# Kernel optimization log

Hardware: AMD Instinct MI355X
Metric: run time of the kernel (lower is better)

Reference implementation:

```python
import jax, jax.numpy as jnp
import numpy as np

EPS = 1e-12  # tf.math.l2_normalize epsilon

def _l2_normalize(v, axis):
    sq = jnp.sum(v * v, axis=axis, keepdims=True)
    return v * jax.lax.rsqrt(jnp.maximum(sq, EPS))

def setup_inputs() -> dict:
    key = jax.random.key(0)
    k1, k2, k3 = jax.random.split(key, 3)
    B, H, Wd, Cin, K = 16, 64, 64, 512, 64  # K == dim (required by the source's broadcast)
    x = jax.random.normal(k1, (B, H, Wd, Cin), dtype=jnp.float32)
    W = jax.random.normal(k2, (Cin, K), dtype=jnp.float32) * (1.0 / np.sqrt(Cin))
    b = jnp.zeros((K,), dtype=jnp.float32)
    C = jax.random.uniform(k3, (1, 1, 1, K, K), dtype=jnp.float32)  # [1,1,1,dim,clusters]
    return {"x": x, "W": W, "b": b, "C": C}

def reference(x, W, b, C):
    # 1x1 conv: per-pixel linear projection to cluster logits. NOTE: the
    # original code overwrites x with the conv output, so the VLAD residual
    # is built from these logits, not the input features (faithful to source).
    f = jnp.einsum('bhwc,ck->bhwk', x, W) + b            # [B,H,W,K]
    s = jax.nn.softmax(f, axis=-1)                        # soft assignment over clusters
    # a: [B,H,W,1,K], residual: [B,H,W,dim,K] with dim==K
    v = s[..., None, :] * (f[..., :, None] + C)           # [B,H,W,dim,K]
    v = jnp.sum(v, axis=(1, 2))                           # [B,dim,K]
    v = jnp.transpose(v, (0, 2, 1))                       # [B,K,dim]
    # postnorm=True: intra-normalize per cluster, then global L2 of flattened
    v = _l2_normalize(v, axis=-1)
    flat = v.reshape(v.shape[0], -1)                      # [B, K*dim]
    return _l2_normalize(flat, axis=-1)
```

## Files before the change

### kernel.cpp

```cpp
#include <hip/hip_runtime.h>
#include <hip/hip_bf16.h>

#define NB 16
#define HW 4096
#define CIN 512
#define KCL 64
#define BP 128
#define NCHUNK 32
#define PSTRIDE 136

typedef short s16x8 __attribute__((ext_vector_type(8)));
typedef int   i32x4 __attribute__((ext_vector_type(4)));
typedef float f32x4 __attribute__((ext_vector_type(4)));

__device__ __forceinline__ unsigned short f2bf(float f) {
    unsigned u = __builtin_bit_cast(unsigned, f);
    u += 0x7fffu + ((u >> 16) & 1u);
    return (unsigned short)(u >> 16);
}

__device__ __forceinline__ unsigned pk2(float lo, float hi) {
    __hip_bfloat162 h = __float22bfloat162_rn(make_float2(lo, hi));
    unsigned r;
    __builtin_memcpy(&r, &h, 4);
    return r;
}

__global__ void vlad_prep(const float* __restrict__ Wm, float* __restrict__ A_g,
                          unsigned short* __restrict__ Wt_g)
{
    const int i = blockIdx.x * 256 + threadIdx.x;
    if (i < NB * KCL * KCL + NB * KCL) A_g[i] = 0.f;
    if (i < CIN * KCL) {
        const int c = i >> 6;
        const int n = i & 63;
        Wt_g[n * 512 + c] = f2bf(Wm[i]);
    }
}

__global__ __launch_bounds__(256, 4) void vlad_main(
    const float* __restrict__ x, const unsigned short* __restrict__ Wt_g,
    const float* __restrict__ bv, float* __restrict__ A_g,
    float* __restrict__ sumS_g)
{
    __shared__ unsigned short ft[KCL * PSTRIDE];
    __shared__ unsigned short st[KCL * PSTRIDE];

    const int t = threadIdx.x;
    const int b = blockIdx.x >> 5;
    const int chunk = blockIdx.x & 31;
    const int pb = b * HW + chunk * BP;

    const int wid = t >> 6;
    const int lane = t & 63;
    const int col = lane & 15;
    const int g = lane >> 4;
    const int wpix = pb + wid * 32;

    f32x4 acc[2][4];
#pragma unroll
    for (int mt = 0; mt < 2; ++mt)
#pragma unroll
        for (int nt = 0; nt < 4; ++nt) acc[mt][nt] = (f32x4){0.f, 0.f, 0.f, 0.f};

    const float* xr0 = x + (size_t)(wpix + col) * CIN + g * 8;
    const float* xr1 = xr0 + 16 * CIN;
    const unsigned short* wbase = Wt_g + col * 512 + g * 8;

#pragma unroll
    for (int kk = 0; kk < 16; ++kk) {
        const int k0 = kk * 32;
        const float4 u00 = *(const float4*)(xr0 + k0);
        const float4 u01 = *(const float4*)(xr0 + k0 + 4);
        const float4 u10 = *(const float4*)(xr1 + k0);
        const float4 u11 = *(const float4*)(xr1 + k0 + 4);
        s16x8 wf[4];
#pragma unroll
        for (int nt = 0; nt < 4; ++nt)
            wf[nt] = *(const s16x8*)(wbase + nt * (16 * 512) + k0);
        const i32x4 a0i = {(int)pk2(u00.x, u00.y), (int)pk2(u00.z, u00.w),
                           (int)pk2(u01.x, u01.y), (int)pk2(u01.z, u01.w)};
        const i32x4 a1i = {(int)pk2(u10.x, u10.y), (int)pk2(u10.z, u10.w),
                           (int)pk2(u11.x, u11.y), (int)pk2(u11.z, u11.w)};
        const s16x8 a0 = __builtin_bit_cast(s16x8, a0i);
        const s16x8 a1 = __builtin_bit_cast(s16x8, a1i);
#pragma unroll
        for (int nt = 0; nt < 4; ++nt) {
            acc[0][nt] = __builtin_amdgcn_mfma_f32_16x16x32_bf16(a0, wf[nt], acc[0][nt], 0, 0, 0);
            acc[1][nt] = __builtin_amdgcn_mfma_f32_16x16x32_bf16(a1, wf[nt], acc[1][nt], 0, 0, 0);
        }
    }

    float bj[4];
#pragma unroll
    for (int nt = 0; nt < 4; ++nt) bj[nt] = bv[nt * 16 + col];
    float ssum[4] = {0.f, 0.f, 0.f, 0.f};

#pragma unroll
    for (int mt = 0; mt < 2; ++mt)
#pragma unroll
        for (int r = 0; r < 4; ++r) {
            float v0 = acc[mt][0][r] + bj[0];
            float v1 = acc[mt][1][r] + bj[1];
            float v2 = acc[mt][2][r] + bj[2];
            float v3 = acc[mt][3][r] + bj[3];
            float m = fmaxf(fmaxf(v0, v1), fmaxf(v2, v3));
            m = fmaxf(m, __shfl_xor(m, 1));
            m = fmaxf(m, __shfl_xor(m, 2));
            m = fmaxf(m, __shfl_xor(m, 4));
            m = fmaxf(m, __shfl_xor(m, 8));
            const float e0 = __expf(v0 - m);
            const float e1 = __expf(v1 - m);
            const float e2 = __expf(v2 - m);
            const float e3 = __expf(v3 - m);
            float lsum = e0 + e1 + e2 + e3;
            lsum += __shfl_xor(lsum, 1);
            lsum += __shfl_xor(lsum, 2);
            lsum += __shfl_xor(lsum, 4);
            lsum += __shfl_xor(lsum, 8);
            const float rl = 1.0f / lsum;
            const float s0 = e0 * rl, s1 = e1 * rl, s2 = e2 * rl, s3 = e3 * rl;
            ssum[0] += s0; ssum[1] += s1; ssum[2] += s2; ssum[3] += s3;
            const int p = wid * 32 + mt * 16 + g * 4 + r;
            ft[(col)      * PSTRIDE + p] = f2bf(v0);
            ft[(col + 16) * PSTRIDE + p] = f2bf(v1);
            ft[(col + 32) * PSTRIDE + p] = f2bf(v2);
            ft[(col + 48) * PSTRIDE + p] = f2bf(v3);
            st[(col)      * PSTRIDE + p] = f2bf(s0);
            st[(col + 16) * PSTRIDE + p] = f2bf(s1);
            st[(col + 32) * PSTRIDE + p] = f2bf(s2);
            st[(col + 48) * PSTRIDE + p] = f2bf(s3);
        }

#pragma unroll
    for (int nt = 0; nt < 4; ++nt) {
        ssum[nt] += __shfl_xor(ssum[nt], 16);
        ssum[nt] += __shfl_xor(ssum[nt], 32);
    }
    if (g == 0) {
#pragma unroll
        for (int nt = 0; nt < 4; ++nt)
            atomicAdd(sumS_g + b * KCL + nt * 16 + col, ssum[nt]);
    }
    __syncthreads();

    f32x4 acc2[4];
#pragma unroll
    for (int nt = 0; nt < 4; ++nt) acc2[nt] = (f32x4){0.f, 0.f, 0.f, 0.f};

    const unsigned short* fta = ft + (wid * 16 + col) * PSTRIDE + g * 8;
#pragma unroll
    for (int kk = 0; kk < 4; ++kk) {
        const s16x8 af = *(const s16x8*)(fta + kk * 32);
#pragma unroll
        for (int nt = 0; nt < 4; ++nt) {
            const s16x8 bf = *(const s16x8*)(st + (nt * 16 + col) * PSTRIDE + kk * 32 + g * 8);
            acc2[nt] = __builtin_amdgcn_mfma_f32_16x16x32_bf16(af, bf, acc2[nt], 0, 0, 0);
        }
    }

    float* Ab = A_g + b * (KCL * KCL);
#pragma unroll
    for (int nt = 0; nt < 4; ++nt)
#pragma unroll
        for (int r = 0; r < 4; ++r)
            atomicAdd(Ab + (wid * 16 + g * 4 + r) * KCL + nt * 16 + col, acc2[nt][r]);
}

__global__ __launch_bounds__(256) void vlad_finalize(
    const float* __restrict__ A_g, const float* __restrict__ sumS_g,
    const float* __restrict__ Cm, float* __restrict__ out)
{
    __shared__ float red[4];
    const int b = blockIdx.x;
    const int t = threadIdx.x;
    const int k = t >> 2;
    const int dg = t & 3;
    const float sS = sumS_g[b * 64 + k];
    float v[16];
    float ssq = 0.f;
#pragma unroll
    for (int i = 0; i < 16; ++i) {
        const int d = dg * 16 + i;
        const float val = A_g[((size_t)b * 64 + d) * 64 + k] + Cm[d * 64 + k] * sS;
        v[i] = val;
        ssq += val * val;
    }
    ssq += __shfl_xor(ssq, 1);
    ssq += __shfl_xor(ssq, 2);
    const float rn = rsqrtf(fmaxf(ssq, 1e-12f));
    float gpart = 0.f;
#pragma unroll
    for (int i = 0; i < 16; ++i) {
        v[i] *= rn;
        gpart += v[i] * v[i];
    }
#pragma unroll
    for (int m = 1; m < 64; m <<= 1) gpart += __shfl_xor(gpart, m);
    if ((t & 63) == 0) red[t >> 6] = gpart;
    __syncthreads();
    const float gsq = red[0] + red[1] + red[2] + red[3];
    const float gr = rsqrtf(fmaxf(gsq, 1e-12f));
    float* o = out + (size_t)b * 4096 + k * 64 + dg * 16;
#pragma unroll
    for (int i = 0; i < 16; ++i) o[i] = v[i] * gr;
}

extern "C" void kernel_launch(void* const* d_in, const int* in_sizes, int n_in,
                              void* d_out, int out_size, void* d_ws, size_t ws_size,
                              hipStream_t stream)
{
    const float* x  = (const float*)d_in[0];
    const float* Wm = (const float*)d_in[1];
    const float* bv = (const float*)d_in[2];
    const float* Cm = (const float*)d_in[3];

    float* A_g = (float*)d_ws;
    float* sumS_g = A_g + NB * KCL * KCL;
    unsigned short* Wt_g = (unsigned short*)(sumS_g + NB * KCL);

    const int nz = NB * KCL * KCL + NB * KCL;
    vlad_prep<<<(nz + 255) / 256, 256, 0, stream>>>(Wm, A_g, Wt_g);
    vlad_main<<<NB * NCHUNK, 256, 0, stream>>>(x, Wt_g, bv, A_g, sumS_g);
    vlad_finalize<<<NB, 256, 0, stream>>>(A_g, sumS_g, Cm, (float*)d_out);
}
```

Measured before the change: 208.7 us.

## Halve pixels per block, double grid, and vectorize LDS stores of logits/softmax

Each block now handles 64 pixels instead of 128, so each wave computes one 16-row MFMA tile instead of two and the grid doubles to 1024 blocks. This is meant to raise parallelism and occupancy for the memory-bound projection and cut register use. The per-element bf16 LDS stores are also replaced by packed 8-byte stores. The cost is twice as many global atomicAdds into the per-batch 64x64 accumulator and into sumS.

```diff
diff --git a/kernel.cpp b/kernel.cpp
--- a/kernel.cpp
+++ b/kernel.cpp
@@ -5,9 +5,9 @@
 #define HW 4096
 #define CIN 512
 #define KCL 64
-#define BP 128
-#define NCHUNK 32
-#define PSTRIDE 136
+#define BP 64
+#define NCHUNK 64
+#define PSTRIDE 72
 
 typedef short s16x8 __attribute__((ext_vector_type(8)));
 typedef int   i32x4 __attribute__((ext_vector_type(4)));
@@ -47,24 +47,21 @@
     __shared__ unsigned short st[KCL * PSTRIDE];
 
     const int t = threadIdx.x;
-    const int b = blockIdx.x >> 5;
-    const int chunk = blockIdx.x & 31;
+    const int b = blockIdx.x >> 6;
+    const int chunk = blockIdx.x & 63;
     const int pb = b * HW + chunk * BP;
 
     const int wid = t >> 6;
     const int lane = t & 63;
     const int col = lane & 15;
     const int g = lane >> 4;
-    const int wpix = pb + wid * 32;
-
-    f32x4 acc[2][4];
-#pragma unroll
-    for (int mt = 0; mt < 2; ++mt)
-#pragma unroll
-        for (int nt = 0; nt < 4; ++nt) acc[mt][nt] = (f32x4){0.f, 0.f, 0.f, 0.f};
+    const int wpix = pb + wid * 16;
+
+    f32x4 acc[4];
+#pragma unroll
+    for (int nt = 0; nt < 4; ++nt) acc[nt] = (f32x4){0.f, 0.f, 0.f, 0.f};
 
     const float* xr0 = x + (size_t)(wpix + col) * CIN + g * 8;
-    const float* xr1 = xr0 + 16 * CIN;
     const unsigned short* wbase = Wt_g + col * 512 + g * 8;
 
 #pragma unroll
@@ -72,65 +69,59 @@
         const int k0 = kk * 32;
         const float4 u00 = *(const float4*)(xr0 + k0);
         const float4 u01 = *(const float4*)(xr0 + k0 + 4);
-        const float4 u10 = *(const float4*)(xr1 + k0);
-        const float4 u11 = *(const float4*)(xr1 + k0 + 4);
         s16x8 wf[4];
 #pragma unroll
         for (int nt = 0; nt < 4; ++nt)
             wf[nt] = *(const s16x8*)(wbase + nt * (16 * 512) + k0);
         const i32x4 a0i = {(int)pk2(u00.x, u00.y), (int)pk2(u00.z, u00.w),
                            (int)pk2(u01.x, u01.y), (int)pk2(u01.z, u01.w)};
-        const i32x4 a1i = {(int)pk2(u10.x, u10.y), (int)pk2(u10.z, u10.w),
-                           (int)pk2(u11.x, u11.y), (int)pk2(u11.z, u11.w)};
         const s16x8 a0 = __builtin_bit_cast(s16x8, a0i);
-        const s16x8 a1 = __builtin_bit_cast(s16x8, a1i);
-#pragma unroll
-        for (int nt = 0; nt < 4; ++nt) {
-            acc[0][nt] = __builtin_amdgcn_mfma_f32_16x16x32_bf16(a0, wf[nt], acc[0][nt], 0, 0, 0);
-            acc[1][nt] = __builtin_amdgcn_mfma_f32_16x16x32_bf16(a1, wf[nt], acc[1][nt], 0, 0, 0);
-        }
+#pragma unroll
+        for (int nt = 0; nt < 4; ++nt)
+            acc[nt] = __builtin_amdgcn_mfma_f32_16x16x32_bf16(a0, wf[nt], acc[nt], 0, 0, 0);
     }
 
     float bj[4];
 #pragma unroll
     for (int nt = 0; nt < 4; ++nt) bj[nt] = bv[nt * 16 + col];
     float ssum[4] = {0.f, 0.f, 0.f, 0.f};
-
-#pragma unroll
-    for (int mt = 0; mt < 2; ++mt)
-#pragma unroll
-        for (int r = 0; r < 4; ++r) {
-            float v0 = acc[mt][0][r] + bj[0];
-            float v1 = acc[mt][1][r] + bj[1];
-            float v2 = acc[mt][2][r] + bj[2];
-            float v3 = acc[mt][3][r] + bj[3];
-            float m = fmaxf(fmaxf(v0, v1), fmaxf(v2, v3));
-            m = fmaxf(m, __shfl_xor(m, 1));
-            m = fmaxf(m, __shfl_xor(m, 2));
-            m = fmaxf(m, __shfl_xor(m, 4));
-            m = fmaxf(m, __shfl_xor(m, 8));
-            const float e0 = __expf(v0 - m);
-            const float e1 = __expf(v1 - m);
-            const float e2 = __expf(v2 - m);
-            const float e3 = __expf(v3 - m);
-            float lsum = e0 + e1 + e2 + e3;
-            lsum += __shfl_xor(lsum, 1);
-            lsum += __shfl_xor(lsum, 2);
-            lsum += __shfl_xor(lsum, 4);
-            lsum += __shfl_xor(lsum, 8);
-            const float rl = 1.0f / lsum;
-            const float s0 = e0 * rl, s1 = e1 * rl, s2 = e2 * rl, s3 = e3 * rl;
-            ssum[0] += s0; ssum[1] += s1; ssum[2] += s2; ssum[3] += s3;
-            const int p = wid * 32 + mt * 16 + g * 4 + r;
-            ft[(col)      * PSTRIDE + p] = f2bf(v0);
-            ft[(col + 16) * PSTRIDE + p] = f2bf(v1);
-            ft[(col + 32) * PSTRIDE + p] = f2bf(v2);
-            ft[(col + 48) * PSTRIDE + p] = f2bf(v3);
-            st[(col)      * PSTRIDE + p] = f2bf(s0);
-            st[(col + 16) * PSTRIDE + p] = f2bf(s1);
-            st[(col + 32) * PSTRIDE + p] = f2bf(s2);
-            st[(col + 48) * PSTRIDE + p] = f2bf(s3);
-        }
+    float fv[4][4], sv[4][4];
+
+#pragma unroll
+    for (int r = 0; r < 4; ++r) {
+        float v0 = acc[0][r] + bj[0];
+        float v1 = acc[1][r] + bj[1];
+        float v2 = acc[2][r] + bj[2];
+        float v3 = acc[3][r] + bj[3];
+        float m = fmaxf(fmaxf(v0, v1), fmaxf(v2, v3));
+        m = fmaxf(m, __shfl_xor(m, 1));
+        m = fmaxf(m, __shfl_xor(m, 2));
+        m = fmaxf(m, __shfl_xor(m, 4));
+        m = fmaxf(m, __shfl_xor(m, 8));
+        const float e0 = __expf(v0 - m);
+        const float e1 = __expf(v1 - m);
+        const float e2 = __expf(v2 - m);
+        const float e3 = __expf(v3 - m);
+        float lsum = e0 + e1 + e2 + e3;
+        lsum += __shfl_xor(lsum, 1);
+        lsum += __shfl_xor(lsum, 2);
+        lsum += __shfl_xor(lsum, 4);
+        lsum += __shfl_xor(lsum, 8);
+        const float rl = 1.0f / lsum;
+        fv[0][r] = v0; fv[1][r] = v1; fv[2][r] = v2; fv[3][r] = v3;
+        sv[0][r] = e0 * rl; sv[1][r] = e1 * rl; sv[2][r] = e2 * rl; sv[3][r] = e3 * rl;
+        ssum[0] += sv[0][r]; ssum[1] += sv[1][r]; ssum[2] += sv[2][r]; ssum[3] += sv[3][r];
+    }
+
+    const int pbase = wid * 16 + g * 4;
+#pragma unroll
+    for (int nt = 0; nt < 4; ++nt) {
+        uint2 fw, sw;
+        fw.x = pk2(fv[nt][0], fv[nt][1]); fw.y = pk2(fv[nt][2], fv[nt][3]);
+        sw.x = pk2(sv[nt][0], sv[nt][1]); sw.y = pk2(sv[nt][2], sv[nt][3]);
+        *(uint2*)(ft + (nt * 16 + col) * PSTRIDE + pbase) = fw;
+        *(uint2*)(st + (nt * 16 + col) * PSTRIDE + pbase) = sw;
+    }
 
 #pragma unroll
     for (int nt = 0; nt < 4; ++nt) {
@@ -150,7 +141,7 @@
 
     const unsigned short* fta = ft + (wid * 16 + col) * PSTRIDE + g * 8;
 #pragma unroll
-    for (int kk = 0; kk < 4; ++kk) {
+    for (int kk = 0; kk < 2; ++kk) {
         const s16x8 af = *(const s16x8*)(fta + kk * 32);
 #pragma unroll
         for (int nt = 0; nt < 4; ++nt) {
```

Result: slower. 223.2 us (+6.9%).

## Stage bf16 weights in LDS, prefetch x ahead, vectorize f/s tile stores

Applied to the files above, without the earlier changes.

Copies the whole bf16 transposed weight matrix into padded shared memory once per block instead of reading it from global memory for every k-step, aliasing that buffer with the later f/s tiles. Adds a 4-deep register prefetch ring for the x float4 loads so global loads run ahead of the MFMAs. Packs the logits and softmax values into bf16 pairs and writes them with 8-byte stores after a barrier. It lowers the occupancy hint from 4 to 2 blocks per CU because shared memory grows to about 65 KB and register pressure rises.

```diff
diff --git a/kernel.cpp b/kernel.cpp
--- a/kernel.cpp
+++ b/kernel.cpp
@@ -7,7 +7,8 @@
 #define KCL 64
 #define BP 128
 #define NCHUNK 32
-#define PSTRIDE 136
+#define PSTR_W 520
+#define PSTR_P 136
 
 typedef short s16x8 __attribute__((ext_vector_type(8)));
 typedef int   i32x4 __attribute__((ext_vector_type(4)));
@@ -38,13 +39,15 @@
     }
 }
 
-__global__ __launch_bounds__(256, 4) void vlad_main(
+__global__ __launch_bounds__(256, 2) void vlad_main(
     const float* __restrict__ x, const unsigned short* __restrict__ Wt_g,
     const float* __restrict__ bv, float* __restrict__ A_g,
     float* __restrict__ sumS_g)
 {
-    __shared__ unsigned short ft[KCL * PSTRIDE];
-    __shared__ unsigned short st[KCL * PSTRIDE];
+    __shared__ unsigned short smem[KCL * PSTR_W];
+    unsigned short* wt = smem;
+    unsigned short* ft = smem;
+    unsigned short* st = smem + KCL * PSTR_P;
 
     const int t = threadIdx.x;
     const int b = blockIdx.x >> 5;
@@ -55,7 +58,15 @@
     const int lane = t & 63;
     const int col = lane & 15;
     const int g = lane >> 4;
-    const int wpix = pb + wid * 32;
+
+#pragma unroll
+    for (int i = 0; i < 16; ++i) {
+        const int idx = i * 256 + t;
+        const int row = idx >> 6;
+        const int c8 = (idx & 63) << 3;
+        *(s16x8*)(wt + row * PSTR_W + c8) = *(const s16x8*)(Wt_g + row * 512 + c8);
+    }
+    __syncthreads();
 
     f32x4 acc[2][4];
 #pragma unroll
@@ -63,21 +74,35 @@
 #pragma unroll
         for (int nt = 0; nt < 4; ++nt) acc[mt][nt] = (f32x4){0.f, 0.f, 0.f, 0.f};
 
-    const float* xr0 = x + (size_t)(wpix + col) * CIN + g * 8;
-    const float* xr1 = xr0 + 16 * CIN;
-    const unsigned short* wbase = Wt_g + col * 512 + g * 8;
+    const float* xp0 = x + (size_t)(pb + wid * 32 + col) * CIN + g * 8;
+    const float* xp1 = xp0 + 16 * CIN;
+    const unsigned short* wb = wt + col * PSTR_W + g * 8;
+
+    float4 xb[4][4];
+#pragma unroll
+    for (int s = 0; s < 4; ++s) {
+        xb[s][0] = *(const float4*)(xp0 + s * 32);
+        xb[s][1] = *(const float4*)(xp0 + s * 32 + 4);
+        xb[s][2] = *(const float4*)(xp1 + s * 32);
+        xb[s][3] = *(const float4*)(xp1 + s * 32 + 4);
+    }
 
 #pragma unroll
     for (int kk = 0; kk < 16; ++kk) {
+        const int s = kk & 3;
+        const float4 u00 = xb[s][0], u01 = xb[s][1];
+        const float4 u10 = xb[s][2], u11 = xb[s][3];
+        if (kk < 12) {
+            xb[s][0] = *(const float4*)(xp0 + (kk + 4) * 32);
+            xb[s][1] = *(const float4*)(xp0 + (kk + 4) * 32 + 4);
+            xb[s][2] = *(const float4*)(xp1 + (kk + 4) * 32);
+            xb[s][3] = *(const float4*)(xp1 + (kk + 4) * 32 + 4);
+        }
         const int k0 = kk * 32;
-        const float4 u00 = *(const float4*)(xr0 + k0);
-        const float4 u01 = *(const float4*)(xr0 + k0 + 4);
-        const float4 u10 = *(const float4*)(xr1 + k0);
-        const float4 u11 = *(const float4*)(xr1 + k0 + 4);
         s16x8 wf[4];
 #pragma unroll
         for (int nt = 0; nt < 4; ++nt)
-            wf[nt] = *(const s16x8*)(wbase + nt * (16 * 512) + k0);
+            wf[nt] = *(const s16x8*)(wb + nt * (16 * PSTR_W) + k0);
         const i32x4 a0i = {(int)pk2(u00.x, u00.y), (int)pk2(u00.z, u00.w),
                            (int)pk2(u01.x, u01.y), (int)pk2(u01.z, u01.w)};
         const i32x4 a1i = {(int)pk2(u10.x, u10.y), (int)pk2(u10.z, u10.w),
@@ -95,9 +120,11 @@
 #pragma unroll
     for (int nt = 0; nt < 4; ++nt) bj[nt] = bv[nt * 16 + col];
     float ssum[4] = {0.f, 0.f, 0.f, 0.f};
-
-#pragma unroll
-    for (int mt = 0; mt < 2; ++mt)
+    uint2 fw[2][4], sw[2][4];
+
+#pragma unroll
+    for (int mt = 0; mt < 2; ++mt) {
+        float fvs[4][4], svs[4][4];
 #pragma unroll
         for (int r = 0; r < 4; ++r) {
             float v0 = acc[mt][0][r] + bj[0];
@@ -119,18 +146,31 @@
             lsum += __shfl_xor(lsum, 4);
             lsum += __shfl_xor(lsum, 8);
             const float rl = 1.0f / lsum;
-            const float s0 = e0 * rl, s1 = e1 * rl, s2 = e2 * rl, s3 = e3 * rl;
-            ssum[0] += s0; ssum[1] += s1; ssum[2] += s2; ssum[3] += s3;
-            const int p = wid * 32 + mt * 16 + g * 4 + r;
-            ft[(col)      * PSTRIDE + p] = f2bf(v0);
-            ft[(col + 16) * PSTRIDE + p] = f2bf(v1);
-            ft[(col + 32) * PSTRIDE + p] = f2bf(v2);
-            ft[(col + 48) * PSTRIDE + p] = f2bf(v3);
-            st[(col)      * PSTRIDE + p] = f2bf(s0);
-            st[(col + 16) * PSTRIDE + p] = f2bf(s1);
-            st[(col + 32) * PSTRIDE + p] = f2bf(s2);
-            st[(col + 48) * PSTRIDE + p] = f2bf(s3);
-        }
+            fvs[0][r] = v0; fvs[1][r] = v1; fvs[2][r] = v2; fvs[3][r] = v3;
+            svs[0][r] = e0 * rl; svs[1][r] = e1 * rl; svs[2][r] = e2 * rl; svs[3][r] = e3 * rl;
+            ssum[0] += svs[0][r]; ssum[1] += svs[1][r];
+            ssum[2] += svs[2][r]; ssum[3] += svs[3][r];
+        }
+#pragma unroll
+        for (int nt = 0; nt < 4; ++nt) {
+            fw[mt][nt].x = pk2(fvs[nt][0], fvs[nt][1]);
+            fw[mt][nt].y = pk2(fvs[nt][2], fvs[nt][3]);
+            sw[mt][nt].x = pk2(svs[nt][0], svs[nt][1]);
+            sw[mt][nt].y = pk2(svs[nt][2], svs[nt][3]);
+        }
+    }
+
+    __syncthreads();
+
+#pragma unroll
+    for (int mt = 0; mt < 2; ++mt) {
+        const int pbase = wid * 32 + mt * 16 + g * 4;
+#pragma unroll
+        for (int nt = 0; nt < 4; ++nt) {
+            *(uint2*)(ft + (nt * 16 + col) * PSTR_P + pbase) = fw[mt][nt];
+            *(uint2*)(st + (nt * 16 + col) * PSTR_P + pbase) = sw[mt][nt];
+        }
+    }
 
 #pragma unroll
     for (int nt = 0; nt < 4; ++nt) {
@@ -148,13 +188,13 @@
 #pragma unroll
     for (int nt = 0; nt < 4; ++nt) acc2[nt] = (f32x4){0.f, 0.f, 0.f, 0.f};
 
-    const unsigned short* fta = ft + (wid * 16 + col) * PSTRIDE + g * 8;
+    const unsigned short* fta = ft + (wid * 16 + col) * PSTR_P + g * 8;
 #pragma unroll
     for (int kk = 0; kk < 4; ++kk) {
         const s16x8 af = *(const s16x8*)(fta + kk * 32);
 #pragma unroll
         for (int nt = 0; nt < 4; ++nt) {
-            const s16x8 bf = *(const s16x8*)(st + (nt * 16 + col) * PSTRIDE + kk * 32 + g * 8);
+            const s16x8 bf = *(const s16x8*)(st + (nt * 16 + col) * PSTR_P + kk * 32 + g * 8);
             acc2[nt] = __builtin_amdgcn_mfma_f32_16x16x32_bf16(af, bf, acc2[nt], 0, 0, 0);
         }
     }
```

Measured after the change: 209.4 us. No clear change (+0.3%).
